# Optimization experiments

Measured on AMD Instinct MI355X. Metric: run time of the kernel, lower is better.

The kernel has to match this reference:

```python
import jax, jax.numpy as jnp
import numpy as np

B, S, D, H = 4, 4096, 1024, 16
HD = D // H  # head_dim = 64

def setup_inputs() -> dict:
    key = jax.random.key(0)
    ks = jax.random.split(key, 9)
    sc = 1.0 / np.sqrt(D)
    return {
        "x": jax.random.normal(ks[0], (B, S, D), dtype=jnp.float32),
        "q_w": jax.random.normal(ks[1], (D, D), dtype=jnp.float32) * sc,
        "q_b": jax.random.normal(ks[2], (D,), dtype=jnp.float32) * 0.01,
        "k_w": jax.random.normal(ks[3], (D, D), dtype=jnp.float32) * sc,
        "k_b": jax.random.normal(ks[4], (D,), dtype=jnp.float32) * 0.01,
        "v_w": jax.random.normal(ks[5], (D, D), dtype=jnp.float32) * sc,
        "v_b": jax.random.normal(ks[6], (D,), dtype=jnp.float32) * 0.01,
        "o_w": jax.random.normal(ks[7], (D, D), dtype=jnp.float32) * sc,
        "o_b": jax.random.normal(ks[8], (D,), dtype=jnp.float32) * 0.01,
    }

def reference(x, q_w, q_b, k_w, k_b, v_w, v_b, o_w, o_b):
    b, s, _ = x.shape
    # Linear projections (torch Linear: x @ W.T + b), split heads
    q = (x @ q_w.T + q_b).reshape(b, s, H, HD)
    k = (x @ k_w.T + k_b).reshape(b, s, H, HD)
    v = (x @ v_w.T + v_b).reshape(b, s, H, HD)
    # ReLU feature map on q and k
    q = jax.nn.relu(q)
    k = jax.nn.relu(k)
    # Non-causal linear attention: kv state then query readout
    kv = jnp.einsum('bshd,bshe->bhde', k, v)   # [B,H,HD,HD]
    out = jnp.einsum('bqhd,bhde->bqhe', q, kv)  # [B,S,H,HD]
    out = out.reshape(b, s, D)
    return out @ o_w.T + o_b
```

## Files before the change

### kernel.cpp

```cpp
#include <hip/hip_runtime.h>

typedef unsigned short ushort_t;
typedef __attribute__((ext_vector_type(8))) __bf16 bf16x8;
typedef __attribute__((ext_vector_type(4))) float f32x4;

#define GLOAD_LDS16(gp, lp)                                                              \
  __builtin_amdgcn_global_load_lds(                                                     \
      (const __attribute__((address_space(1))) unsigned int*)(gp),                      \
      (__attribute__((address_space(3))) unsigned int*)(lp), 16, 0, 0)

#define MEMFENCE() asm volatile("" ::: "memory")
#define SBARRIER()                          \
  do {                                      \
    MEMFENCE();                             \
    __builtin_amdgcn_s_barrier();           \
    MEMFENCE();                             \
  } while (0)
#define WAIT_LGKM0()                                     \
  do {                                                   \
    asm volatile("s_waitcnt lgkmcnt(0)" ::: "memory");   \
    __builtin_amdgcn_sched_barrier(0);                   \
  } while (0)
#define WAIT_VM2() asm volatile("s_waitcnt vmcnt(2)" ::: "memory")

__device__ __forceinline__ ushort_t f2bf(float f) {
  unsigned u = __builtin_bit_cast(unsigned, f);
  u += 0x7fffu + ((u >> 16) & 1u);
  return (ushort_t)(u >> 16);
}
__device__ __forceinline__ float bf2f(ushort_t h) {
  return __builtin_bit_cast(float, (unsigned)h << 16);
}

__global__ __launch_bounds__(256) void k_f32_to_bf16(const float* __restrict__ src,
                                                     ushort_t* __restrict__ dst, int n) {
  int i = (blockIdx.x * 256 + threadIdx.x) * 4;
  if (i >= n) return;
  float4 v = *reinterpret_cast<const float4*>(src + i);
  ushort4 o;
  o.x = f2bf(v.x); o.y = f2bf(v.y); o.z = f2bf(v.z); o.w = f2bf(v.w);
  *reinterpret_cast<ushort4*>(dst + i) = o;
}

__global__ __launch_bounds__(256) void k_pack_w4(const float* __restrict__ w0,
                                                 const float* __restrict__ w1,
                                                 const float* __restrict__ w2,
                                                 const float* __restrict__ w3,
                                                 ushort_t* __restrict__ dst) {
  const int blk = blockIdx.x;
  const int wsel = blk >> 10;
  const float* src = wsel == 0 ? w0 : wsel == 1 ? w1 : wsel == 2 ? w2 : w3;
  const int off = (blk & 1023) * 1024 + threadIdx.x * 4;
  float4 v = *reinterpret_cast<const float4*>(src + off);
  ushort4 o;
  o.x = f2bf(v.x); o.y = f2bf(v.y); o.z = f2bf(v.z); o.w = f2bf(v.w);
  *reinterpret_cast<ushort4*>(dst + wsel * 1048576 + off) = o;
}


__device__ __forceinline__ void stage_half(const ushort_t* __restrict__ g, int ld, int kt,
                                           ushort_t* slot, int w, int lane) {
  const int swz = ((lane & 7) ^ (lane >> 3)) * 8;
#pragma unroll
  for (int l = 0; l < 2; l++) {
    int row = l * 64 + w * 8 + (lane >> 3);
    GLOAD_LDS16(g + (long)row * ld + kt + swz, slot + l * 4096 + w * 512);
  }
}

__device__ __forceinline__ bf16x8 read_frag(const ushort_t* slot, int row, int kbyte) {
  int byte = row * 128 + (kbyte ^ ((row & 7) << 4));
  return *reinterpret_cast<const bf16x8*>(reinterpret_cast<const char*>(slot) + byte);
}

template <bool OUT_F32>
__global__ __launch_bounds__(512, 2) void k_gemm256(
    const ushort_t* __restrict__ A, int lda, long strideA,
    const ushort_t* __restrict__ Bw, int ldb, long strideB,
    const float* __restrict__ bias, int relu_lim,
    void* __restrict__ Cout, int ldc, long strideC, int K) {
  __shared__ ushort_t lds[65536];
  const int t = threadIdx.x;
  const int lane = t & 63;
  const int w = t >> 6;
  const int wm = w >> 2, wn = w & 3;
  const int z = blockIdx.z;

  const int nx = gridDim.x;
  const int nwg = nx * gridDim.y;
  const int lin = blockIdx.x + blockIdx.y * nx;
  const int q8 = nwg >> 3;
  const int s = (lin & 7) * q8 + (lin >> 3);
  const long rowBase = (long)(s / nx) * 256;
  const long colBase = (long)(s % nx) * 256;

  const ushort_t* Ap = A + z * strideA + rowBase * lda;
  const ushort_t* Bp = Bw + z * strideB + colBase * ldb;

#define SLOT(buf, isB, half) (lds + (buf) * 32768 + (isB) * 16384 + (half) * 8192)
#define STAGE(gb, ld, kt, buf, isB, half) stage_half((gb), (ld), (kt), SLOT(buf, isB, half), w, lane)

  f32x4 acc[8][4];
#pragma unroll
  for (int mi = 0; mi < 8; mi++)
#pragma unroll
    for (int ni = 0; ni < 4; ni++) acc[mi][ni] = (f32x4){0.f, 0.f, 0.f, 0.f};
  bf16x8 Ar[4][2], Br[4][2];
  const int fr = lane & 15;
  const int kb = (lane >> 4) * 16;

#define LOADA(buf, miB)                                                             \
  do {                                                                              \
    const ushort_t* sl = SLOT(buf, 0, wm);                                          \
    _Pragma("unroll") for (int mi = 0; mi < 4; mi++)                                \
        _Pragma("unroll") for (int ks = 0; ks < 2; ks++)                            \
            Ar[mi][ks] = read_frag(sl, (miB + mi) * 16 + fr, ks * 64 + kb);         \
  } while (0)
#define LOADB(buf, ns)                                                              \
  do {                                                                              \
    const ushort_t* sl = SLOT(buf, 1, wn >> 1);                                     \
    _Pragma("unroll") for (int nj = 0; nj < 2; nj++)                                \
        _Pragma("unroll") for (int ks = 0; ks < 2; ks++)                            \
            Br[(ns) * 2 + nj][ks] =                                                 \
                read_frag(sl, (wn & 1) * 64 + ((ns) * 2 + nj) * 16 + fr, ks * 64 + kb); \
  } while (0)
#define MFMA16(miB, ns)                                                             \
  do {                                                                              \
    _Pragma("unroll") for (int ks = 0; ks < 2; ks++)                                \
        _Pragma("unroll") for (int mi = 0; mi < 4; mi++)                            \
            _Pragma("unroll") for (int nj = 0; nj < 2; nj++)                        \
                acc[(miB) + mi][(ns) * 2 + nj] = __builtin_amdgcn_mfma_f32_16x16x32_bf16( \
                    Ar[mi][ks], Br[(ns) * 2 + nj][ks], acc[(miB) + mi][(ns) * 2 + nj], 0, 0, 0); \
  } while (0)

  const ushort_t* Ap1 = Ap + 128 * (long)lda;
  const ushort_t* Bp1 = Bp + 128 * (long)ldb;

  STAGE(Ap, lda, 0, 0, 0, 0);
  STAGE(Bp, ldb, 0, 0, 1, 0);
  STAGE(Ap1, lda, 0, 0, 0, 1);
  STAGE(Bp1, ldb, 0, 0, 1, 1);
  STAGE(Ap, lda, 64, 1, 0, 0);
  WAIT_VM2();
  SBARRIER();

  const int NT2 = K >> 7;
  for (int it = 0; it < NT2; it++) {
    const int kt = it << 7;
    const int ktb = kt + 64;
    const int ktn = (kt + 128 < K) ? kt + 128 : K - 64;
    const int ktn2 = (kt + 192 < K) ? kt + 192 : K - 64;

    LOADA(0, 0); LOADB(0, 0);
    STAGE(Bp, ldb, ktb, 1, 1, 0);
    SBARRIER(); WAIT_LGKM0();
    __builtin_amdgcn_s_setprio(1); MFMA16(0, 0); __builtin_amdgcn_s_setprio(0);
    SBARRIER();
    LOADB(0, 1);
    STAGE(Ap1, lda, ktb, 1, 0, 1);
    SBARRIER(); WAIT_LGKM0();
    __builtin_amdgcn_s_setprio(1); MFMA16(0, 1); __builtin_amdgcn_s_setprio(0);
    SBARRIER();
    LOADA(0, 4);
    STAGE(Bp1, ldb, ktb, 1, 1, 1);
    SBARRIER(); WAIT_LGKM0();
    __builtin_amdgcn_s_setprio(1); MFMA16(4, 0); __builtin_amdgcn_s_setprio(0);
    SBARRIER();
    STAGE(Ap, lda, ktn, 0, 0, 0);
    SBARRIER(); WAIT_LGKM0();
    __builtin_amdgcn_s_setprio(1); MFMA16(4, 1); __builtin_amdgcn_s_setprio(0);
    WAIT_VM2();
    SBARRIER();
    LOADA(1, 0); LOADB(1, 0);
    STAGE(Bp, ldb, ktn, 0, 1, 0);
    SBARRIER(); WAIT_LGKM0();
    __builtin_amdgcn_s_setprio(1); MFMA16(0, 0); __builtin_amdgcn_s_setprio(0);
    SBARRIER();
    LOADB(1, 1);
    STAGE(Ap1, lda, ktn, 0, 0, 1);
    SBARRIER(); WAIT_LGKM0();
    __builtin_amdgcn_s_setprio(1); MFMA16(0, 1); __builtin_amdgcn_s_setprio(0);
    SBARRIER();
    LOADA(1, 4);
    STAGE(Bp1, ldb, ktn, 0, 1, 1);
    SBARRIER(); WAIT_LGKM0();
    __builtin_amdgcn_s_setprio(1); MFMA16(4, 0); __builtin_amdgcn_s_setprio(0);
    SBARRIER();
    STAGE(Ap, lda, ktn2, 1, 0, 0);
    SBARRIER(); WAIT_LGKM0();
    __builtin_amdgcn_s_setprio(1); MFMA16(4, 1); __builtin_amdgcn_s_setprio(0);
    WAIT_VM2();
    SBARRIER();
  }

  const int rowQ = (lane >> 4) * 4;
#pragma unroll
  for (int ni = 0; ni < 4; ni++) {
    const int col = (int)colBase + wn * 64 + ni * 16 + fr;
    const float bv = bias[col];
    const bool doRelu = col < relu_lim;
#pragma unroll
    for (int mi = 0; mi < 8; mi++) {
      const long row = rowBase + wm * 128 + mi * 16 + rowQ;
#pragma unroll
      for (int r = 0; r < 4; r++) {
        float v = acc[mi][ni][r] + bv;
        if (doRelu) v = fmaxf(v, 0.f);
        if (OUT_F32)
          ((float*)Cout)[z * strideC + (row + r) * (long)ldc + col] = v;
        else
          ((ushort_t*)Cout)[z * strideC + (row + r) * (long)ldc + col] = f2bf(v);
      }
    }
  }
#undef SLOT
#undef STAGE
#undef LOADA
#undef LOADB
#undef MFMA16
}

__global__ __launch_bounds__(64) void k_kv_partial(const ushort_t* __restrict__ qkv,
                                                   float* __restrict__ partial) {
  const int bh = blockIdx.x;
  const int chunk = blockIdx.y;
  const int b = bh >> 4, h = bh & 15;
  const int t = threadIdx.x;
  const int d0 = (t >> 2) * 4;
  const int e0 = (t & 3) * 16;
  __shared__ float kk[16][64];
  __shared__ float vv[16][64];
  float acc[4][16];
#pragma unroll
  for (int di = 0; di < 4; di++)
#pragma unroll
    for (int j = 0; j < 16; j++) acc[di][j] = 0.f;

  const long rowbase = (long)b * 4096 + (long)chunk * 128;
  for (int it = 0; it < 8; it++) {
    __syncthreads();
#pragma unroll
    for (int rep = 0; rep < 4; rep++) {
      int idx = rep * 64 + t;
      int row = idx >> 4, c4 = (idx & 15) * 4;
      long m = rowbase + it * 16 + row;
      ushort4 kr = *reinterpret_cast<const ushort4*>(&qkv[m * 3072 + 1024 + h * 64 + c4]);
      ushort4 vr = *reinterpret_cast<const ushort4*>(&qkv[m * 3072 + 2048 + h * 64 + c4]);
      float4 kf = make_float4(bf2f(kr.x), bf2f(kr.y), bf2f(kr.z), bf2f(kr.w));
      float4 vf = make_float4(bf2f(vr.x), bf2f(vr.y), bf2f(vr.z), bf2f(vr.w));
      *reinterpret_cast<float4*>(&kk[row][c4]) = kf;
      *reinterpret_cast<float4*>(&vv[row][c4]) = vf;
    }
    __syncthreads();
#pragma unroll
    for (int ss = 0; ss < 16; ss++) {
      const float4 kq = *reinterpret_cast<const float4*>(&kk[ss][d0]);
#pragma unroll
      for (int jj = 0; jj < 4; jj++) {
        const float4 vq = *reinterpret_cast<const float4*>(&vv[ss][e0 + jj * 4]);
        acc[0][jj * 4 + 0] = fmaf(kq.x, vq.x, acc[0][jj * 4 + 0]);
        acc[0][jj * 4 + 1] = fmaf(kq.x, vq.y, acc[0][jj * 4 + 1]);
        acc[0][jj * 4 + 2] = fmaf(kq.x, vq.z, acc[0][jj * 4 + 2]);
        acc[0][jj * 4 + 3] = fmaf(kq.x, vq.w, acc[0][jj * 4 + 3]);
        acc[1][jj * 4 + 0] = fmaf(kq.y, vq.x, acc[1][jj * 4 + 0]);
        acc[1][jj * 4 + 1] = fmaf(kq.y, vq.y, acc[1][jj * 4 + 1]);
        acc[1][jj * 4 + 2] = fmaf(kq.y, vq.z, acc[1][jj * 4 + 2]);
        acc[1][jj * 4 + 3] = fmaf(kq.y, vq.w, acc[1][jj * 4 + 3]);
        acc[2][jj * 4 + 0] = fmaf(kq.z, vq.x, acc[2][jj * 4 + 0]);
        acc[2][jj * 4 + 1] = fmaf(kq.z, vq.y, acc[2][jj * 4 + 1]);
        acc[2][jj * 4 + 2] = fmaf(kq.z, vq.z, acc[2][jj * 4 + 2]);
        acc[2][jj * 4 + 3] = fmaf(kq.z, vq.w, acc[2][jj * 4 + 3]);
        acc[3][jj * 4 + 0] = fmaf(kq.w, vq.x, acc[3][jj * 4 + 0]);
        acc[3][jj * 4 + 1] = fmaf(kq.w, vq.y, acc[3][jj * 4 + 1]);
        acc[3][jj * 4 + 2] = fmaf(kq.w, vq.z, acc[3][jj * 4 + 2]);
        acc[3][jj * 4 + 3] = fmaf(kq.w, vq.w, acc[3][jj * 4 + 3]);
      }
    }
  }
  float* dst = partial + ((long)chunk * 64 + bh) * 4096;
#pragma unroll
  for (int di = 0; di < 4; di++)
#pragma unroll
    for (int jj = 0; jj < 4; jj++) {
      float4 o = make_float4(acc[di][jj * 4], acc[di][jj * 4 + 1], acc[di][jj * 4 + 2],
                             acc[di][jj * 4 + 3]);
      *reinterpret_cast<float4*>(&dst[(d0 + di) * 64 + e0 + jj * 4]) = o;
    }
}

__global__ __launch_bounds__(256) void k_kv_reduce(const float* __restrict__ partial,
                                                   float* __restrict__ kv) {
  int i4 = (blockIdx.x * 256 + threadIdx.x) * 4;
  float4 s = make_float4(0.f, 0.f, 0.f, 0.f);
#pragma unroll
  for (int c = 0; c < 32; c++) {
    float4 p = *reinterpret_cast<const float4*>(&partial[(long)c * 262144 + i4]);
    s.x += p.x; s.y += p.y; s.z += p.z; s.w += p.w;
  }
  *reinterpret_cast<float4*>(&kv[i4]) = s;
}

__global__ __launch_bounds__(256) void k_fuse_w(const float* __restrict__ kv,
                                                const ushort_t* __restrict__ ow,
                                                ushort_t* __restrict__ qkv) {
  const int nt = blockIdx.x;
  const int h = blockIdx.y;
  const int b = blockIdx.z;
  const int t = threadIdx.x;
  const int nn = t >> 2;
  const int d0 = (t & 3) * 16;
  __shared__ float kvt[64][68];
  __shared__ ushort_t ows[64][68];
  const float* kvsrc = kv + (long)(b * 16 + h) * 4096;
  const int n0 = nt * 64;
#pragma unroll
  for (int rep = 0; rep < 16; rep++) {
    int lin = rep * 256 + t;
    int d = lin >> 6, e = lin & 63;
    kvt[e][d] = kvsrc[d * 64 + e];
  }
#pragma unroll
  for (int rep = 0; rep < 4; rep++) {
    int lin = rep * 256 + t;
    int r = lin >> 4, c4 = (lin & 15) * 4;
    *reinterpret_cast<ushort4*>(&ows[r][c4]) =
        *reinterpret_cast<const ushort4*>(&ow[(long)(n0 + r) * 1024 + h * 64 + c4]);
  }
  __syncthreads();
  float acc[16];
#pragma unroll
  for (int j = 0; j < 16; j++) acc[j] = 0.f;
  for (int e = 0; e < 64; e++) {
    float own = bf2f(ows[nn][e]);
#pragma unroll
    for (int jj = 0; jj < 4; jj++) {
      const float4 kq = *reinterpret_cast<const float4*>(&kvt[e][d0 + jj * 4]);
      acc[jj * 4 + 0] = fmaf(own, kq.x, acc[jj * 4 + 0]);
      acc[jj * 4 + 1] = fmaf(own, kq.y, acc[jj * 4 + 1]);
      acc[jj * 4 + 2] = fmaf(own, kq.z, acc[jj * 4 + 2]);
      acc[jj * 4 + 3] = fmaf(own, kq.w, acc[jj * 4 + 3]);
    }
  }
  ushort_t* dst = qkv + (long)(b * 1024 + n0 + nn) * 3072 + 1024 + h * 64 + d0;
#pragma unroll
  for (int jj = 0; jj < 4; jj++) {
    ushort4 o;
    o.x = f2bf(acc[jj * 4 + 0]); o.y = f2bf(acc[jj * 4 + 1]);
    o.z = f2bf(acc[jj * 4 + 2]); o.w = f2bf(acc[jj * 4 + 3]);
    *reinterpret_cast<ushort4*>(dst + jj * 4) = o;
  }
}

extern "C" void kernel_launch(void* const* d_in, const int* in_sizes, int n_in, void* d_out,
                              int out_size, void* d_ws, size_t ws_size, hipStream_t stream) {
  const float* x   = (const float*)d_in[0];
  const float* q_w = (const float*)d_in[1];
  const float* q_b = (const float*)d_in[2];
  const float* k_w = (const float*)d_in[3];
  const float* k_b = (const float*)d_in[4];
  const float* v_w = (const float*)d_in[5];
  const float* v_b = (const float*)d_in[6];
  const float* o_w = (const float*)d_in[7];
  const float* o_b = (const float*)d_in[8];
  float* out = (float*)d_out;

  const int D = 1024, M = 16384;
  char* ws = (char*)d_ws;
  ushort_t* xb    = (ushort_t*)(ws);
  ushort_t* wqkv  = (ushort_t*)(ws + 33554432);
  ushort_t* owb   = (ushort_t*)(ws + 39845888);
  float*    biasq = (float*)(ws + 41943040);
  ushort_t* qkv   = (ushort_t*)(ws + 41955328);
  float* partial = (float*)(ws);
  float* kvbuf   = (float*)(ws + 33554432);

  k_f32_to_bf16<<<16384, 256, 0, stream>>>(x, xb, M * D);
  k_pack_w4<<<4096, 256, 0, stream>>>(q_w, k_w, v_w, o_w, wqkv);
  hipMemcpyAsync(biasq, q_b, D * sizeof(float), hipMemcpyDeviceToDevice, stream);
  hipMemcpyAsync(biasq + D, k_b, D * sizeof(float), hipMemcpyDeviceToDevice, stream);
  hipMemcpyAsync(biasq + 2 * D, v_b, D * sizeof(float), hipMemcpyDeviceToDevice, stream);

  k_gemm256<false><<<dim3(12, 64, 1), 512, 0, stream>>>(xb, 1024, 0, wqkv, 1024, 0,
                                                        biasq, 2048, qkv, 3072, 0, 1024);
  k_kv_partial<<<dim3(64, 32), 64, 0, stream>>>(qkv, partial);
  k_kv_reduce<<<256, 256, 0, stream>>>(partial, kvbuf);
  k_fuse_w<<<dim3(16, 16, 4), 256, 0, stream>>>(kvbuf, owb, qkv);
  k_gemm256<true><<<dim3(4, 16, 4), 512, 0, stream>>>(
      qkv, 3072, (long)4096 * 3072, qkv + 1024, 3072, (long)1024 * 3072,
      o_b, 0, out, 1024, (long)4096 * 1024, 1024);
}
```

Measured before the change: 243.5 us.

## Stage GEMM epilogue through LDS for vectorized stores, drop explicit LDS waits, fuse bias copies

The GEMM epilogue now writes each 16-row accumulator slab into per-wave LDS scratch and reads it back as contiguous rows. Global stores become 16-byte vector stores instead of scattered scalar ones. The main loop drops the explicit lgkmcnt(0) waits, moves the second B fragment load earlier, and leaves LDS-read ordering to the compiler. The three device-to-device bias memcpys become a single small kernel launch. Removing the manual waits risks relying on compiler-inserted waits, and reusing the LDS tile buffer in the epilogue needs the final barrier to be correct.

```diff
diff --git a/kernel.cpp b/kernel.cpp
--- a/kernel.cpp
+++ b/kernel.cpp
@@ -2,6 +2,7 @@
 
 typedef unsigned short ushort_t;
 typedef __attribute__((ext_vector_type(8))) __bf16 bf16x8;
+typedef __attribute__((ext_vector_type(8))) unsigned short us8;
 typedef __attribute__((ext_vector_type(4))) float f32x4;
 
 #define GLOAD_LDS16(gp, lp)                                                              \
@@ -16,12 +17,8 @@
     __builtin_amdgcn_s_barrier();           \
     MEMFENCE();                             \
   } while (0)
-#define WAIT_LGKM0()                                     \
-  do {                                                   \
-    asm volatile("s_waitcnt lgkmcnt(0)" ::: "memory");   \
-    __builtin_amdgcn_sched_barrier(0);                   \
-  } while (0)
 #define WAIT_VM2() asm volatile("s_waitcnt vmcnt(2)" ::: "memory")
+#define WAIT_VM0() asm volatile("s_waitcnt vmcnt(0)" ::: "memory")
 
 __device__ __forceinline__ ushort_t f2bf(float f) {
   unsigned u = __builtin_bit_cast(unsigned, f);
@@ -55,6 +52,15 @@
   ushort4 o;
   o.x = f2bf(v.x); o.y = f2bf(v.y); o.z = f2bf(v.z); o.w = f2bf(v.w);
   *reinterpret_cast<ushort4*>(dst + wsel * 1048576 + off) = o;
+}
+
+__global__ __launch_bounds__(256) void k_pack_bias(const float* __restrict__ q_b,
+                                                   const float* __restrict__ k_b,
+                                                   const float* __restrict__ v_b,
+                                                   float* __restrict__ biasq) {
+  int i = blockIdx.x * 256 + threadIdx.x;
+  const float* s = i < 1024 ? q_b : (i < 2048 ? k_b : v_b);
+  biasq[i] = s[i & 1023];
 }
 
 
@@ -151,66 +157,93 @@
     const int ktn = (kt + 128 < K) ? kt + 128 : K - 64;
     const int ktn2 = (kt + 192 < K) ? kt + 192 : K - 64;
 
-    LOADA(0, 0); LOADB(0, 0);
+    LOADA(0, 0); LOADB(0, 0); LOADB(0, 1);
     STAGE(Bp, ldb, ktb, 1, 1, 0);
-    SBARRIER(); WAIT_LGKM0();
+    SBARRIER();
     __builtin_amdgcn_s_setprio(1); MFMA16(0, 0); __builtin_amdgcn_s_setprio(0);
     SBARRIER();
-    LOADB(0, 1);
     STAGE(Ap1, lda, ktb, 1, 0, 1);
-    SBARRIER(); WAIT_LGKM0();
+    SBARRIER();
     __builtin_amdgcn_s_setprio(1); MFMA16(0, 1); __builtin_amdgcn_s_setprio(0);
     SBARRIER();
     LOADA(0, 4);
     STAGE(Bp1, ldb, ktb, 1, 1, 1);
-    SBARRIER(); WAIT_LGKM0();
+    SBARRIER();
     __builtin_amdgcn_s_setprio(1); MFMA16(4, 0); __builtin_amdgcn_s_setprio(0);
     SBARRIER();
     STAGE(Ap, lda, ktn, 0, 0, 0);
-    SBARRIER(); WAIT_LGKM0();
+    SBARRIER();
     __builtin_amdgcn_s_setprio(1); MFMA16(4, 1); __builtin_amdgcn_s_setprio(0);
     WAIT_VM2();
     SBARRIER();
-    LOADA(1, 0); LOADB(1, 0);
+    LOADA(1, 0); LOADB(1, 0); LOADB(1, 1);
     STAGE(Bp, ldb, ktn, 0, 1, 0);
-    SBARRIER(); WAIT_LGKM0();
+    SBARRIER();
     __builtin_amdgcn_s_setprio(1); MFMA16(0, 0); __builtin_amdgcn_s_setprio(0);
     SBARRIER();
-    LOADB(1, 1);
     STAGE(Ap1, lda, ktn, 0, 0, 1);
-    SBARRIER(); WAIT_LGKM0();
+    SBARRIER();
     __builtin_amdgcn_s_setprio(1); MFMA16(0, 1); __builtin_amdgcn_s_setprio(0);
     SBARRIER();
     LOADA(1, 4);
     STAGE(Bp1, ldb, ktn, 0, 1, 1);
-    SBARRIER(); WAIT_LGKM0();
+    SBARRIER();
     __builtin_amdgcn_s_setprio(1); MFMA16(4, 0); __builtin_amdgcn_s_setprio(0);
     SBARRIER();
     STAGE(Ap, lda, ktn2, 1, 0, 0);
-    SBARRIER(); WAIT_LGKM0();
+    SBARRIER();
     __builtin_amdgcn_s_setprio(1); MFMA16(4, 1); __builtin_amdgcn_s_setprio(0);
     WAIT_VM2();
     SBARRIER();
   }
 
-  const int rowQ = (lane >> 4) * 4;
-#pragma unroll
-  for (int ni = 0; ni < 4; ni++) {
-    const int col = (int)colBase + wn * 64 + ni * 16 + fr;
-    const float bv = bias[col];
-    const bool doRelu = col < relu_lim;
+  WAIT_VM0();
+  SBARRIER();
+  {
+    float* sl = reinterpret_cast<float*>(lds) + w * 2048;
+    const int rowQ = (lane >> 4) * 4;
+    float bv[4];
+#pragma unroll
+    for (int ni = 0; ni < 4; ni++) bv[ni] = bias[(int)colBase + wn * 64 + ni * 16 + fr];
+    const int rr = lane >> 2;
+    const int cq = (lane & 3) * 16;
 #pragma unroll
     for (int mi = 0; mi < 8; mi++) {
-      const long row = rowBase + wm * 128 + mi * 16 + rowQ;
-#pragma unroll
-      for (int r = 0; r < 4; r++) {
-        float v = acc[mi][ni][r] + bv;
-        if (doRelu) v = fmaxf(v, 0.f);
-        if (OUT_F32)
-          ((float*)Cout)[z * strideC + (row + r) * (long)ldc + col] = v;
-        else
-          ((ushort_t*)Cout)[z * strideC + (row + r) * (long)ldc + col] = f2bf(v);
+#pragma unroll
+      for (int ni = 0; ni < 4; ni++) {
+        const bool doRelu = ((int)colBase + wn * 64 + ni * 16 + fr) < relu_lim;
+#pragma unroll
+        for (int r = 0; r < 4; r++) {
+          float v = acc[mi][ni][r] + bv[ni];
+          if (doRelu) v = fmaxf(v, 0.f);
+          sl[(rowQ + r) * 68 + ni * 16 + fr] = v;
+        }
       }
+      asm volatile("s_waitcnt lgkmcnt(0)" ::: "memory");
+      __builtin_amdgcn_sched_barrier(0);
+      float4 v0 = *reinterpret_cast<const float4*>(&sl[rr * 68 + cq]);
+      float4 v1 = *reinterpret_cast<const float4*>(&sl[rr * 68 + cq + 4]);
+      float4 v2 = *reinterpret_cast<const float4*>(&sl[rr * 68 + cq + 8]);
+      float4 v3 = *reinterpret_cast<const float4*>(&sl[rr * 68 + cq + 12]);
+      const long row = rowBase + wm * 128 + mi * 16 + rr;
+      const long gc = colBase + wn * 64 + cq;
+      if (OUT_F32) {
+        float* dst = (float*)Cout + z * strideC + row * (long)ldc + gc;
+        *reinterpret_cast<float4*>(dst) = v0;
+        *reinterpret_cast<float4*>(dst + 4) = v1;
+        *reinterpret_cast<float4*>(dst + 8) = v2;
+        *reinterpret_cast<float4*>(dst + 12) = v3;
+      } else {
+        ushort_t* dst = (ushort_t*)Cout + z * strideC + row * (long)ldc + gc;
+        us8 o0, o1;
+        o0[0] = f2bf(v0.x); o0[1] = f2bf(v0.y); o0[2] = f2bf(v0.z); o0[3] = f2bf(v0.w);
+        o0[4] = f2bf(v1.x); o0[5] = f2bf(v1.y); o0[6] = f2bf(v1.z); o0[7] = f2bf(v1.w);
+        o1[0] = f2bf(v2.x); o1[1] = f2bf(v2.y); o1[2] = f2bf(v2.z); o1[3] = f2bf(v2.w);
+        o1[4] = f2bf(v3.x); o1[5] = f2bf(v3.y); o1[6] = f2bf(v3.z); o1[7] = f2bf(v3.w);
+        *reinterpret_cast<us8*>(dst) = o0;
+        *reinterpret_cast<us8*>(dst + 8) = o1;
+      }
+      asm volatile("s_waitcnt lgkmcnt(0)" ::: "memory");
     }
   }
 #undef SLOT
@@ -376,9 +409,7 @@
 
   k_f32_to_bf16<<<16384, 256, 0, stream>>>(x, xb, M * D);
   k_pack_w4<<<4096, 256, 0, stream>>>(q_w, k_w, v_w, o_w, wqkv);
-  hipMemcpyAsync(biasq, q_b, D * sizeof(float), hipMemcpyDeviceToDevice, stream);
-  hipMemcpyAsync(biasq + D, k_b, D * sizeof(float), hipMemcpyDeviceToDevice, stream);
-  hipMemcpyAsync(biasq + 2 * D, v_b, D * sizeof(float), hipMemcpyDeviceToDevice, stream);
+  k_pack_bias<<<12, 256, 0, stream>>>(q_b, k_b, v_b, biasq);
 
   k_gemm256<false><<<dim3(12, 64, 1), 512, 0, stream>>>(xb, 1024, 0, wqkv, 1024, 0,
                                                         biasq, 2048, qkv, 3072, 0, 1024);
```

After: 245.0 us. About the same (+0.6%).
